# Kernel optimization log

Hardware: AMD Instinct MI355X
Metric: run time of the kernel (lower is better)

The kernel has to match this reference:

```python
import jax, jax.numpy as jnp
import numpy as np

NCLASS = 19


def setup_inputs() -> dict:
    key = jax.random.key(0)
    k1, k2 = jax.random.split(key)
    logits = jax.random.normal(k1, (4, NCLASS, 512, 1024), dtype=jnp.float32)
    target = jax.random.randint(k2, (4, 512, 1024), 0, NCLASS, dtype=jnp.int32)
    return {"logits": logits, "target": target}


def reference(logits, target):
    # Faithful to the torch module: per predicted class cls,
    #   cls_vectors    = logits values at all (c, pixel) positions whose
    #                    argmax-predicted class == cls, grouped per sample n
    #   cls_prototype  = scalar mean of those values per sample
    #   cls_center_loss = mean_n || cls_vectors_n - prototype_n ||_2
    # and the total loss sums over classes. The Python loop + boolean masked
    # select is replaced by one fused segmented reduction using the identity
    #   sum((x - m)^2) = S2 - S1^2 / K   with m = S1/K.
    N, C, H, W = logits.shape
    probs = jax.nn.softmax(logits, axis=1)
    preds = jnp.argmax(probs, axis=1)              # (N, H, W) int

    x = logits.reshape(N, C, H * W)
    s1 = jnp.sum(x, axis=1).reshape(-1)            # (N*HW,) sum over channels per pixel
    s2 = jnp.sum(x * x, axis=1).reshape(-1)        # (N*HW,)
    ones = jnp.ones_like(s1)

    # segment id = sample index * C + predicted class  -> N*C segments
    seg = (preds.reshape(N, -1) + jnp.arange(N, dtype=preds.dtype)[:, None] * C).reshape(-1)
    data = jnp.stack([s1, s2, ones], axis=-1)      # (N*HW, 3)
    sums = jax.ops.segment_sum(data, seg, num_segments=N * C)  # (N*C, 3)
    sums = sums.reshape(N, C, 3)
    S1, S2, cnt = sums[..., 0], sums[..., 1], sums[..., 2]      # (N, nclass)

    # each matching pixel contributes C values => K = cnt * C elements per (n, cls)
    K = jnp.maximum(cnt, 1.0) * C
    sq_dev = jnp.maximum(S2 - S1 * S1 / K, 0.0)    # sum of squared deviations
    norms = jnp.where(cnt > 0, jnp.sqrt(sq_dev), 0.0)           # (N, nclass)

    center_loss = jnp.sum(jnp.mean(norms, axis=0))  # sum over classes of mean over N
    return center_loss
```

## Files before the change

kernel.cpp:

```cpp
#include <hip/hip_runtime.h>

#define NCLS 19
#define NSMP 4
#define HW   (512 * 1024)
#define NSEG (NSMP * NCLS)

__global__ void cl_init_ws(float* ws) {
    int i = threadIdx.x;
    if (i < 3 * NSEG) ws[i] = 0.0f;
}

__global__ __launch_bounds__(256) void cl_main(const float* __restrict__ logits,
                                               float* __restrict__ ws) {
    __shared__ float sS1[NCLS];
    __shared__ float sS2[NCLS];
    __shared__ float sCnt[NCLS];
    const int tid = threadIdx.x;
    if (tid < NCLS) { sS1[tid] = 0.0f; sS2[tid] = 0.0f; sCnt[tid] = 0.0f; }
    __syncthreads();

    const long long p   = ((long long)blockIdx.x * 256 + tid) * 4;
    const int       n   = (int)(p / HW);
    const long long off = p - (long long)n * HW;
    const float* base = logits + (size_t)n * NCLS * HW + off;

    float4 v[NCLS];
    #pragma unroll
    for (int c = 0; c < NCLS; ++c) {
        v[c] = *(const float4*)(base + (size_t)c * HW);
    }
    asm volatile("" ::: "memory");

    float s1[4], s2[4], mv[4];
    int   mi[4];
    {
        const float a0[4] = {v[0].x, v[0].y, v[0].z, v[0].w};
        #pragma unroll
        for (int j = 0; j < 4; ++j) {
            s1[j] = a0[j];
            s2[j] = a0[j] * a0[j];
            mv[j] = a0[j];
            mi[j] = 0;
        }
    }
    #pragma unroll
    for (int c = 1; c < NCLS; ++c) {
        const float a[4] = {v[c].x, v[c].y, v[c].z, v[c].w};
        #pragma unroll
        for (int j = 0; j < 4; ++j) {
            s1[j] += a[j];
            s2[j] += a[j] * a[j];
            if (a[j] > mv[j]) { mv[j] = a[j]; mi[j] = c; }
        }
    }

    #pragma unroll
    for (int j = 0; j < 4; ++j) {
        atomicAdd(&sS1[mi[j]],  s1[j]);
        atomicAdd(&sS2[mi[j]],  s2[j]);
        atomicAdd(&sCnt[mi[j]], 1.0f);
    }
    __syncthreads();

    if (tid < NCLS) {
        const int seg = n * NCLS + tid;
        atomicAdd(&ws[seg],            sS1[tid]);
        atomicAdd(&ws[NSEG + seg],     sS2[tid]);
        atomicAdd(&ws[2 * NSEG + seg], sCnt[tid]);
    }
}

__global__ void cl_final(const float* __restrict__ ws, float* __restrict__ out) {
    __shared__ float red[128];
    const int i = threadIdx.x;
    float v = 0.0f;
    if (i < NSEG) {
        const float S1  = ws[i];
        const float S2  = ws[NSEG + i];
        const float cnt = ws[2 * NSEG + i];
        const float K   = fmaxf(cnt, 1.0f) * (float)NCLS;
        const float sq  = fmaxf(S2 - S1 * S1 / K, 0.0f);
        v = (cnt > 0.0f) ? sqrtf(sq) : 0.0f;
    }
    red[i] = v;
    __syncthreads();
    #pragma unroll
    for (int s = 64; s > 0; s >>= 1) {
        if (i < s) red[i] += red[i + s];
        __syncthreads();
    }
    if (i == 0) out[0] = red[0] / (float)NSMP;
}

extern "C" void kernel_launch(void* const* d_in, const int* in_sizes, int n_in,
                              void* d_out, int out_size, void* d_ws, size_t ws_size,
                              hipStream_t stream) {
    const float* logits = (const float*)d_in[0];
    float* ws  = (float*)d_ws;
    float* out = (float*)d_out;

    cl_init_ws<<<1, 256, 0, stream>>>(ws);

    const long long total_pixels = (long long)NSMP * HW;
    const int blocks = (int)(total_pixels / 4 / 256);
    cl_main<<<blocks, 256, 0, stream>>>(logits, ws);

    cl_final<<<1, 128, 0, stream>>>(ws, out);
}
```

Baseline: 55.28 us.

## Replace global atomics with per-block partials and a wave-shuffle final reduction

Result: slower. 66.16 us (+19.7%).

```diff
diff --git a/kernel.cpp b/kernel.cpp
--- a/kernel.cpp
+++ b/kernel.cpp
@@ -3,20 +3,15 @@
 #define NCLS 19
 #define NSMP 4
 #define HW   (512 * 1024)
-#define NSEG (NSMP * NCLS)
-
-__global__ void cl_init_ws(float* ws) {
-    int i = threadIdx.x;
-    if (i < 3 * NSEG) ws[i] = 0.0f;
-}
+#define NVAL 57
+#define PSTRIDE 64
+#define NBLK 2048
 
 __global__ __launch_bounds__(256) void cl_main(const float* __restrict__ logits,
-                                               float* __restrict__ ws) {
-    __shared__ float sS1[NCLS];
-    __shared__ float sS2[NCLS];
-    __shared__ float sCnt[NCLS];
+                                               float* __restrict__ partials) {
+    __shared__ float sb[NVAL];
     const int tid = threadIdx.x;
-    if (tid < NCLS) { sS1[tid] = 0.0f; sS2[tid] = 0.0f; sCnt[tid] = 0.0f; }
+    if (tid < NVAL) sb[tid] = 0.0f;
     __syncthreads();
 
     const long long p   = ((long long)blockIdx.x * 256 + tid) * 4;
@@ -49,61 +44,78 @@
         #pragma unroll
         for (int j = 0; j < 4; ++j) {
             s1[j] += a[j];
-            s2[j] += a[j] * a[j];
+            s2[j]  = fmaf(a[j], a[j], s2[j]);
             if (a[j] > mv[j]) { mv[j] = a[j]; mi[j] = c; }
         }
     }
 
     #pragma unroll
     for (int j = 0; j < 4; ++j) {
-        atomicAdd(&sS1[mi[j]],  s1[j]);
-        atomicAdd(&sS2[mi[j]],  s2[j]);
-        atomicAdd(&sCnt[mi[j]], 1.0f);
+        atomicAdd(&sb[mi[j]],      s1[j]);
+        atomicAdd(&sb[19 + mi[j]], s2[j]);
+        atomicAdd(&sb[38 + mi[j]], 1.0f);
     }
     __syncthreads();
 
-    if (tid < NCLS) {
-        const int seg = n * NCLS + tid;
-        atomicAdd(&ws[seg],            sS1[tid]);
-        atomicAdd(&ws[NSEG + seg],     sS2[tid]);
-        atomicAdd(&ws[2 * NSEG + seg], sCnt[tid]);
+    if (tid < PSTRIDE) {
+        partials[(size_t)blockIdx.x * PSTRIDE + tid] = (tid < NVAL) ? sb[tid] : 0.0f;
     }
 }
 
-__global__ void cl_final(const float* __restrict__ ws, float* __restrict__ out) {
-    __shared__ float red[128];
-    const int i = threadIdx.x;
-    float v = 0.0f;
-    if (i < NSEG) {
-        const float S1  = ws[i];
-        const float S2  = ws[NSEG + i];
-        const float cnt = ws[2 * NSEG + i];
+__global__ __launch_bounds__(256) void cl_final(const float* __restrict__ partials,
+                                                float* __restrict__ out) {
+    const int tid  = threadIdx.x;
+    const int w    = tid >> 6;
+    const int lane = tid & 63;
+
+    float acc[60];
+    #pragma unroll
+    for (int i = 0; i < 60; ++i) acc[i] = 0.0f;
+
+    #pragma unroll
+    for (int k = 0; k < 8; ++k) {
+        const float* row = partials + (size_t)(w * 512 + lane + (k << 6)) * PSTRIDE;
+        #pragma unroll
+        for (int vq = 0; vq < 15; ++vq) {
+            float4 t = *(const float4*)(row + vq * 4);
+            acc[4 * vq + 0] += t.x;
+            acc[4 * vq + 1] += t.y;
+            acc[4 * vq + 2] += t.z;
+            acc[4 * vq + 3] += t.w;
+        }
+    }
+
+    #pragma unroll
+    for (int s = 1; s < 64; s <<= 1) {
+        #pragma unroll
+        for (int i = 0; i < 60; ++i) acc[i] += __shfl_xor(acc[i], s, 64);
+    }
+
+    float loss = 0.0f;
+    if (lane < NCLS) {
+        const float S1  = acc[lane];
+        const float S2  = acc[19 + lane];
+        const float cnt = acc[38 + lane];
         const float K   = fmaxf(cnt, 1.0f) * (float)NCLS;
         const float sq  = fmaxf(S2 - S1 * S1 / K, 0.0f);
-        v = (cnt > 0.0f) ? sqrtf(sq) : 0.0f;
+        loss = (cnt > 0.0f) ? sqrtf(sq) : 0.0f;
     }
-    red[i] = v;
+    #pragma unroll
+    for (int s = 1; s < 32; s <<= 1) loss += __shfl_xor(loss, s, 64);
+
+    __shared__ float L[4];
+    if (lane == 0) L[w] = loss;
     __syncthreads();
-    #pragma unroll
-    for (int s = 64; s > 0; s >>= 1) {
-        if (i < s) red[i] += red[i + s];
-        __syncthreads();
-    }
-    if (i == 0) out[0] = red[0] / (float)NSMP;
+    if (tid == 0) out[0] = (L[0] + L[1] + L[2] + L[3]) * 0.25f;
 }
 
 extern "C" void kernel_launch(void* const* d_in, const int* in_sizes, int n_in,
                               void* d_out, int out_size, void* d_ws, size_t ws_size,
                               hipStream_t stream) {
     const float* logits = (const float*)d_in[0];
-    float* ws  = (float*)d_ws;
-    float* out = (float*)d_out;
+    float* partials = (float*)d_ws;
+    float* out      = (float*)d_out;
 
-    cl_init_ws<<<1, 256, 0, stream>>>(ws);
-
-    const long long total_pixels = (long long)NSMP * HW;
-    const int blocks = (int)(total_pixels / 4 / 256);
-    cl_main<<<blocks, 256, 0, stream>>>(logits, ws);
-
-    cl_final<<<1, 128, 0, stream>>>(ws, out);
+    cl_main<<<NBLK, 256, 0, stream>>>(logits, partials);
+    cl_final<<<1, 256, 0, stream>>>(partials, out);
 }
```

## Use float2 loads with 512-thread blocks and memset-based workspace init

Applied to the files above, without the earlier changes.

New measurement: 57.86 us. 4.7% more time.

```diff
diff --git a/kernel.cpp b/kernel.cpp
--- a/kernel.cpp
+++ b/kernel.cpp
@@ -5,38 +5,30 @@
 #define HW   (512 * 1024)
 #define NSEG (NSMP * NCLS)
 
-__global__ void cl_init_ws(float* ws) {
-    int i = threadIdx.x;
-    if (i < 3 * NSEG) ws[i] = 0.0f;
-}
-
-__global__ __launch_bounds__(256) void cl_main(const float* __restrict__ logits,
-                                               float* __restrict__ ws) {
-    __shared__ float sS1[NCLS];
-    __shared__ float sS2[NCLS];
-    __shared__ float sCnt[NCLS];
+__global__ __launch_bounds__(512, 8) void cl_main(const float* __restrict__ logits,
+                                                  float* __restrict__ ws) {
+    __shared__ float sb[3 * NCLS];
     const int tid = threadIdx.x;
-    if (tid < NCLS) { sS1[tid] = 0.0f; sS2[tid] = 0.0f; sCnt[tid] = 0.0f; }
+    if (tid < 3 * NCLS) sb[tid] = 0.0f;
     __syncthreads();
 
-    const long long p   = ((long long)blockIdx.x * 256 + tid) * 4;
-    const int       n   = (int)(p / HW);
-    const long long off = p - (long long)n * HW;
+    const int    n   = blockIdx.x >> 9;
+    const size_t off = ((size_t)(blockIdx.x & 511)) * 1024 + (size_t)tid * 2;
     const float* base = logits + (size_t)n * NCLS * HW + off;
 
-    float4 v[NCLS];
+    float2 v[NCLS];
     #pragma unroll
     for (int c = 0; c < NCLS; ++c) {
-        v[c] = *(const float4*)(base + (size_t)c * HW);
+        v[c] = *(const float2*)(base + (size_t)c * HW);
     }
     asm volatile("" ::: "memory");
 
-    float s1[4], s2[4], mv[4];
-    int   mi[4];
+    float s1[2], s2[2], mv[2];
+    int   mi[2];
     {
-        const float a0[4] = {v[0].x, v[0].y, v[0].z, v[0].w};
+        const float a0[2] = {v[0].x, v[0].y};
         #pragma unroll
-        for (int j = 0; j < 4; ++j) {
+        for (int j = 0; j < 2; ++j) {
             s1[j] = a0[j];
             s2[j] = a0[j] * a0[j];
             mv[j] = a0[j];
@@ -45,28 +37,28 @@
     }
     #pragma unroll
     for (int c = 1; c < NCLS; ++c) {
-        const float a[4] = {v[c].x, v[c].y, v[c].z, v[c].w};
+        const float a[2] = {v[c].x, v[c].y};
         #pragma unroll
-        for (int j = 0; j < 4; ++j) {
+        for (int j = 0; j < 2; ++j) {
             s1[j] += a[j];
-            s2[j] += a[j] * a[j];
+            s2[j]  = fmaf(a[j], a[j], s2[j]);
             if (a[j] > mv[j]) { mv[j] = a[j]; mi[j] = c; }
         }
     }
 
     #pragma unroll
-    for (int j = 0; j < 4; ++j) {
-        atomicAdd(&sS1[mi[j]],  s1[j]);
-        atomicAdd(&sS2[mi[j]],  s2[j]);
-        atomicAdd(&sCnt[mi[j]], 1.0f);
+    for (int j = 0; j < 2; ++j) {
+        atomicAdd(&sb[mi[j]],      s1[j]);
+        atomicAdd(&sb[19 + mi[j]], s2[j]);
+        atomicAdd(&sb[38 + mi[j]], 1.0f);
     }
     __syncthreads();
 
     if (tid < NCLS) {
         const int seg = n * NCLS + tid;
-        atomicAdd(&ws[seg],            sS1[tid]);
-        atomicAdd(&ws[NSEG + seg],     sS2[tid]);
-        atomicAdd(&ws[2 * NSEG + seg], sCnt[tid]);
+        atomicAdd(&ws[seg],            sb[tid]);
+        atomicAdd(&ws[NSEG + seg],     sb[19 + tid]);
+        atomicAdd(&ws[2 * NSEG + seg], sb[38 + tid]);
     }
 }
 
@@ -99,11 +91,7 @@
     float* ws  = (float*)d_ws;
     float* out = (float*)d_out;
 
-    cl_init_ws<<<1, 256, 0, stream>>>(ws);
-
-    const long long total_pixels = (long long)NSMP * HW;
-    const int blocks = (int)(total_pixels / 4 / 256);
-    cl_main<<<blocks, 256, 0, stream>>>(logits, ws);
-
+    hipMemsetAsync(ws, 0, 3 * NSEG * sizeof(float), stream);
+    cl_main<<<2048, 512, 0, stream>>>(logits, ws);
     cl_final<<<1, 128, 0, stream>>>(ws, out);
 }
```
